# Optimization experiments

Measured on AMD Instinct MI355X. Metric: run time of the kernel, lower is better.

Reference implementation:

```python
import jax, jax.numpy as jnp
import numpy as np

N_NODES = 100_000
N_EDGES = 3_200_000
F_IN, F_HID, F_OUT = 128, 128, 64
BN_EPS = 1e-5


def gcn_conv(x, src, dst, W, b, n_nodes):
    """PyG GCNConv: x' = D^{-1/2}(A+I)D^{-1/2} (x W) + b, self-loops included in src/dst."""
    h = x @ W                                                  # [N, out]
    ones = jnp.ones(src.shape[0], dtype=x.dtype)
    deg = jax.ops.segment_sum(ones, dst, num_segments=n_nodes)  # in-degree incl. self-loop (>=1)
    dinv = jax.lax.rsqrt(deg)
    norm = dinv[src] * dinv[dst]                               # [E+N]
    msg = h[src] * norm[:, None]                               # gather + scale
    out = jax.ops.segment_sum(msg, dst, num_segments=n_nodes)  # scatter-add
    return out + b


def setup_inputs() -> dict:
    key = jax.random.key(0)
    ks = jax.random.split(key, 6)
    x = jax.random.normal(ks[0], (N_NODES, F_IN), dtype=jnp.float32)
    edge_index = jax.random.randint(ks[1], (2, N_EDGES), 0, N_NODES, dtype=jnp.int32)
    W1 = jax.random.normal(ks[2], (F_IN, F_HID), dtype=jnp.float32) / np.sqrt(F_IN)
    b1 = jnp.zeros((F_HID,), dtype=jnp.float32)
    gamma = jnp.ones((F_HID,), dtype=jnp.float32)
    beta = jnp.zeros((F_HID,), dtype=jnp.float32)
    W2 = jax.random.normal(ks[3], (F_HID, F_OUT), dtype=jnp.float32) / np.sqrt(F_HID)
    b2 = jnp.zeros((F_OUT,), dtype=jnp.float32)
    return {"x": x, "edge_index": edge_index, "W1": W1, "b1": b1,
            "gamma": gamma, "beta": beta, "W2": W2, "b2": b2}


def reference(x, edge_index, W1, b1, gamma, beta, W2, b2):
    n = x.shape[0]
    loop = jnp.arange(n, dtype=edge_index.dtype)
    src = jnp.concatenate([edge_index[0], loop])
    dst = jnp.concatenate([edge_index[1], loop])
    # conv1
    h = gcn_conv(x, src, dst, W1, b1, n)
    # BatchNorm1d (training mode: batch stats, biased variance)
    mean = jnp.mean(h, axis=0)
    var = jnp.mean((h - mean) ** 2, axis=0)
    h = (h - mean) * jax.lax.rsqrt(var + BN_EPS) * gamma + beta
    # ReLU
    h = jax.nn.relu(h)
    # conv2
    return gcn_conv(h, src, dst, W2, b2, n)
```

## Files before the change

### kernel.cpp

```cpp
#include <hip/hip_runtime.h>
#include <math.h>


typedef _Float16 f16;
typedef _Float16 f16x2 __attribute__((ext_vector_type(2)));
typedef _Float16 f16x8 __attribute__((ext_vector_type(8)));
typedef float f32x4 __attribute__((ext_vector_type(4)));

static constexpr int KDIM = 128;
static constexpr int MAXNB = 1600;
static constexpr int CAP = 2560;
static constexpr int CHUNK = 8192;
static constexpr int BINT = 512;
static constexpr int WTP = 136;

__global__ __launch_bounds__(BINT) void binA_kernel(
    const int* __restrict__ src, const int* __restrict__ dst, int E,
    int* __restrict__ bcur, unsigned int* __restrict__ bins, int nbuck) {
  __shared__ int hist[MAXNB];
  __shared__ int base[MAXNB];
  const int tid = threadIdx.x;
  for (int b = tid; b < nbuck; b += BINT) hist[b] = 0;
  __syncthreads();
  const int e0 = blockIdx.x * CHUNK;
  const int e1 = min(e0 + CHUNK, E);
  for (int e = e0 + tid * 4; e + 3 < e1; e += BINT * 4) {
    int4 d4 = *reinterpret_cast<const int4*>(&dst[e]);
    atomicAdd(&hist[d4.x >> 6], 1);
    atomicAdd(&hist[d4.y >> 6], 1);
    atomicAdd(&hist[d4.z >> 6], 1);
    atomicAdd(&hist[d4.w >> 6], 1);
  }
  for (int e = e1 - (e1 - e0) % 4 + tid; e < e1; e += BINT) atomicAdd(&hist[dst[e] >> 6], 1);
  __syncthreads();
  for (int b = tid; b < nbuck; b += BINT) {
    int c = hist[b];
    base[b] = c ? atomicAdd(&bcur[b], c) : 0;
    hist[b] = 0;
  }
  __syncthreads();
  for (int e = e0 + tid * 4; e + 3 < e1; e += BINT * 4) {
    int4 d4 = *reinterpret_cast<const int4*>(&dst[e]);
    int4 s4 = *reinterpret_cast<const int4*>(&src[e]);
    int dd[4] = {d4.x, d4.y, d4.z, d4.w};
    int ss[4] = {s4.x, s4.y, s4.z, s4.w};
#pragma unroll
    for (int k = 0; k < 4; ++k) {
      int b = dd[k] >> 6;
      int lp = atomicAdd(&hist[b], 1);
      int p = base[b] + lp;
      if (p < CAP)
        bins[(size_t)b * CAP + p] =
            (unsigned int)ss[k] | ((unsigned int)(dd[k] & 63) << 17);
    }
  }
  for (int e = e1 - (e1 - e0) % 4 + tid; e < e1; e += BINT) {
    int d = dst[e];
    int b = d >> 6;
    int lp = atomicAdd(&hist[b], 1);
    int p = base[b] + lp;
    if (p < CAP)
      bins[(size_t)b * CAP + p] = (unsigned int)src[e] | ((unsigned int)(d & 63) << 17);
  }
}

__global__ __launch_bounds__(1024) void bscan_kernel(
    const int* __restrict__ bcur, int nbuck, int* __restrict__ bbase,
    int* __restrict__ off_n, f16* __restrict__ h1rown) {
  __shared__ int sh[1024];
  const int t = threadIdx.x;
  if (t < 128) h1rown[t] = (f16)0.f;
  int a = (2 * t < nbuck) ? min(bcur[2 * t], CAP) : 0;
  int b = (2 * t + 1 < nbuck) ? min(bcur[2 * t + 1], CAP) : 0;
  sh[t] = a + b;
  __syncthreads();
  for (int o = 1; o < 1024; o <<= 1) {
    int v = (t >= o) ? sh[t - o] : 0;
    __syncthreads();
    sh[t] += v;
    __syncthreads();
  }
  int excl = (t > 0) ? sh[t - 1] : 0;
  if (2 * t < nbuck) bbase[2 * t] = excl;
  if (2 * t + 1 < nbuck) bbase[2 * t + 1] = excl + a;
  if (t == 1023) off_n[0] = sh[1023];
}

__global__ __launch_bounds__(256) void csrfill_kernel(
    const unsigned int* __restrict__ bins, const int* __restrict__ bcur,
    const int* __restrict__ bbase, int* __restrict__ csr, int* __restrict__ off,
    float* __restrict__ dinv, int n) {
  __shared__ int hist[64];
  __shared__ int pref[64];
  __shared__ int lcur[64];
  const int tid = threadIdx.x;
  const int b = blockIdx.x;
  const int cnt = min(bcur[b], CAP);
  const unsigned int* bp = bins + (size_t)b * CAP;
  if (tid < 64) hist[tid] = 0;
  __syncthreads();
  for (int e = tid; e < cnt; e += 256) atomicAdd(&hist[bp[e] >> 17], 1);
  __syncthreads();
  if (tid < 64) pref[tid] = hist[tid];
  __syncthreads();
  for (int o = 1; o < 64; o <<= 1) {
    int v = (tid < 64 && tid >= o) ? pref[tid - o] : 0;
    __syncthreads();
    if (tid < 64) pref[tid] += v;
    __syncthreads();
  }
  if (tid < 64) {
    int node = b * 64 + tid;
    if (node < n) {
      int excl = bbase[b] + pref[tid] - hist[tid];
      off[node] = excl;
      lcur[tid] = excl;
      dinv[node] = rsqrtf((float)(hist[tid] + 1));
    }
  }
  __syncthreads();
  for (int e = tid; e < cnt; e += 256) {
    unsigned int pk = bp[e];
    int r = pk >> 17;
    int p = atomicAdd(&lcur[r], 1);
    csr[p] = (int)(pk & 0x1FFFF);
  }
}

__global__ __launch_bounds__(256) void gemm1_kernel(
    const float* __restrict__ A, const float* __restrict__ W, f16* __restrict__ C,
    int M, const float* __restrict__ dinv) {
  __shared__ f16 Wt[128][WTP];
  const int tid = threadIdx.x;
  for (int idx = tid; idx < 128 * 128; idx += 256) {
    int k = idx >> 7, nn = idx & 127;
    Wt[nn][k] = (f16)W[idx];
  }
  __syncthreads();
  const int wave = tid >> 6;
  const int lane = tid & 63;
  const int r = lane & 15;
  const int kg = lane >> 4;
  const int row0 = blockIdx.x * 64 + wave * 16;
  const bool valid = (row0 + r) < M;
  const float* arow = A + (size_t)(row0 + r) * KDIM;
  f32x4 acc[8];
#pragma unroll
  for (int nf = 0; nf < 8; ++nf) acc[nf] = (f32x4){0.f, 0.f, 0.f, 0.f};
#pragma unroll
  for (int ks = 0; ks < 4; ++ks) {
    const int k0 = ks * 32 + kg * 8;
    f16x8 a;
#pragma unroll
    for (int z = 0; z < 8; ++z) a[z] = (f16)0.f;
    if (valid) {
      float4 u = *reinterpret_cast<const float4*>(arow + k0);
      float4 v = *reinterpret_cast<const float4*>(arow + k0 + 4);
      a[0] = (f16)u.x; a[1] = (f16)u.y; a[2] = (f16)u.z; a[3] = (f16)u.w;
      a[4] = (f16)v.x; a[5] = (f16)v.y; a[6] = (f16)v.z; a[7] = (f16)v.w;
    }
#pragma unroll
    for (int nf = 0; nf < 8; ++nf) {
      f16x8 b = *reinterpret_cast<const f16x8*>(&Wt[nf * 16 + r][k0]);
      acc[nf] = __builtin_amdgcn_mfma_f32_16x16x32_f16(a, b, acc[nf], 0, 0, 0);
    }
  }
  const int crow = row0 + (lane >> 4) * 4;
  const int ccol = lane & 15;
#pragma unroll
  for (int q = 0; q < 4; ++q) {
    int rr = crow + q;
    if (rr < M) {
      float dv = dinv[rr];
#pragma unroll
      for (int nf = 0; nf < 8; ++nf)
        C[(size_t)rr * 128 + nf * 16 + ccol] = (f16)(acc[nf][q] * dv);
    }
  }
}

__global__ __launch_bounds__(256) void gemm2_kernel(
    const f16* __restrict__ A, const float* __restrict__ W, f16* __restrict__ C,
    int M, const float* __restrict__ ss, const float* __restrict__ dinv) {
  __shared__ f16 Wt[64][WTP];
  const int tid = threadIdx.x;
  for (int idx = tid; idx < 128 * 64; idx += 256) {
    int k = idx >> 6, nn = idx & 63;
    Wt[nn][k] = (f16)W[idx];
  }
  __syncthreads();
  const int wave = tid >> 6;
  const int lane = tid & 63;
  const int r = lane & 15;
  const int kg = lane >> 4;
  const int row0 = blockIdx.x * 64 + wave * 16;
  const bool valid = (row0 + r) < M;
  const f16* arow = A + (size_t)(row0 + r) * KDIM;
  f32x4 acc[4];
#pragma unroll
  for (int nf = 0; nf < 4; ++nf) acc[nf] = (f32x4){0.f, 0.f, 0.f, 0.f};
#pragma unroll
  for (int ks = 0; ks < 4; ++ks) {
    const int k0 = ks * 32 + kg * 8;
    f16x8 a;
#pragma unroll
    for (int z = 0; z < 8; ++z) a[z] = (f16)0.f;
    if (valid) {
      f16x8 raw = *reinterpret_cast<const f16x8*>(arow + k0);
      float4 s0 = *reinterpret_cast<const float4*>(&ss[k0]);
      float4 s1 = *reinterpret_cast<const float4*>(&ss[k0 + 4]);
      float4 t0 = *reinterpret_cast<const float4*>(&ss[128 + k0]);
      float4 t1 = *reinterpret_cast<const float4*>(&ss[128 + k0 + 4]);
      a[0] = (f16)fmaxf((float)raw[0] * s0.x + t0.x, 0.f);
      a[1] = (f16)fmaxf((float)raw[1] * s0.y + t0.y, 0.f);
      a[2] = (f16)fmaxf((float)raw[2] * s0.z + t0.z, 0.f);
      a[3] = (f16)fmaxf((float)raw[3] * s0.w + t0.w, 0.f);
      a[4] = (f16)fmaxf((float)raw[4] * s1.x + t1.x, 0.f);
      a[5] = (f16)fmaxf((float)raw[5] * s1.y + t1.y, 0.f);
      a[6] = (f16)fmaxf((float)raw[6] * s1.z + t1.z, 0.f);
      a[7] = (f16)fmaxf((float)raw[7] * s1.w + t1.w, 0.f);
    }
#pragma unroll
    for (int nf = 0; nf < 4; ++nf) {
      f16x8 b = *reinterpret_cast<const f16x8*>(&Wt[nf * 16 + r][k0]);
      acc[nf] = __builtin_amdgcn_mfma_f32_16x16x32_f16(a, b, acc[nf], 0, 0, 0);
    }
  }
  const int crow = row0 + (lane >> 4) * 4;
  const int ccol = lane & 15;
#pragma unroll
  for (int q = 0; q < 4; ++q) {
    int rr = crow + q;
    if (rr < M) {
      float dv = dinv[rr];
#pragma unroll
      for (int nf = 0; nf < 4; ++nf)
        C[(size_t)rr * 64 + nf * 16 + ccol] = (f16)(acc[nf][q] * dv);
    }
  }
}

__global__ __launch_bounds__(64) void agg1_kernel(
    const f16* __restrict__ h, const float* __restrict__ dinv,
    const int* __restrict__ off, const int* __restrict__ csr,
    const float* __restrict__ bias, f16* __restrict__ outh, int n) {
  const int i = blockIdx.x;
  const int t = threadIdx.x;
  const float di = dinv[i];
  const float2 bi = *reinterpret_cast<const float2*>(&bias[2 * t]);
  f16x2 hs = *reinterpret_cast<const f16x2*>(&h[(size_t)i * 128 + 2 * t]);
  float e0 = (float)hs[0];
  float e1 = (float)hs[1];
  const int beg = __builtin_amdgcn_readfirstlane(off[i]);
  const int end = __builtin_amdgcn_readfirstlane(off[i + 1]);
  for (int j = beg & ~15; j < end; j += 16) {
    int4 q0 = *reinterpret_cast<const int4*>(&csr[j]);
    int4 q1 = *reinterpret_cast<const int4*>(&csr[j + 4]);
    int4 q2 = *reinterpret_cast<const int4*>(&csr[j + 8]);
    int4 q3 = *reinterpret_cast<const int4*>(&csr[j + 12]);
    int s[16] = {q0.x, q0.y, q0.z, q0.w, q1.x, q1.y, q1.z, q1.w,
                 q2.x, q2.y, q2.z, q2.w, q3.x, q3.y, q3.z, q3.w};
    if (j < beg || j + 16 > end) {
#pragma unroll
      for (int k = 0; k < 16; ++k)
        if (j + k < beg || j + k >= end) s[k] = n;
    }
    f16x2 v[16];
#pragma unroll
    for (int k = 0; k < 16; ++k)
      v[k] = *reinterpret_cast<const f16x2*>(&h[(size_t)s[k] * 128 + 2 * t]);
#pragma unroll
    for (int k = 0; k < 16; ++k) {
      e0 += (float)v[k][0];
      e1 += (float)v[k][1];
    }
  }
  f16x2 o;
  o[0] = (f16)(di * e0 + bi.x);
  o[1] = (f16)(di * e1 + bi.y);
  *reinterpret_cast<f16x2*>(&outh[(size_t)i * 128 + 2 * t]) = o;
}

__global__ __launch_bounds__(64) void agg2_kernel(
    const f16* __restrict__ h, const float* __restrict__ dinv,
    const int* __restrict__ off, const int* __restrict__ csr,
    const float* __restrict__ bias, float* __restrict__ out, int n) {
  const int i = blockIdx.x;
  const int lane = threadIdx.x;
  const int epar = lane >> 5;
  const int cp = lane & 31;
  const float di = dinv[i];
  float e0 = 0.f, e1 = 0.f;
  const int beg = __builtin_amdgcn_readfirstlane(off[i]);
  const int end = __builtin_amdgcn_readfirstlane(off[i + 1]);
  for (int j = beg & ~15; j < end; j += 16) {
    int4 q0 = *reinterpret_cast<const int4*>(&csr[j]);
    int4 q1 = *reinterpret_cast<const int4*>(&csr[j + 4]);
    int4 q2 = *reinterpret_cast<const int4*>(&csr[j + 8]);
    int4 q3 = *reinterpret_cast<const int4*>(&csr[j + 12]);
    int s[16] = {q0.x, q0.y, q0.z, q0.w, q1.x, q1.y, q1.z, q1.w,
                 q2.x, q2.y, q2.z, q2.w, q3.x, q3.y, q3.z, q3.w};
    if (j < beg || j + 16 > end) {
#pragma unroll
      for (int k = 0; k < 16; ++k)
        if (j + k < beg || j + k >= end) s[k] = n;
    }
#pragma unroll
    for (int k = 0; k < 8; ++k) {
      int se = epar ? s[2 * k + 1] : s[2 * k];
      f16x2 v = *reinterpret_cast<const f16x2*>(&h[(size_t)se * 64 + 2 * cp]);
      e0 += (float)v[0];
      e1 += (float)v[1];
    }
  }
  e0 += __shfl_xor(e0, 32, 64);
  e1 += __shfl_xor(e1, 32, 64);
  if (epar == 0) {
    f16x2 hv = *reinterpret_cast<const f16x2*>(&h[(size_t)i * 64 + 2 * cp]);
    float2 bi = *reinterpret_cast<const float2*>(&bias[2 * cp]);
    float2 o;
    o.x = di * (e0 + (float)hv[0]) + bi.x;
    o.y = di * (e1 + (float)hv[1]) + bi.y;
    *reinterpret_cast<float2*>(&out[(size_t)i * 64 + 2 * cp]) = o;
  }
}

__global__ __launch_bounds__(256) void bnstat_kernel(
    const f16* __restrict__ a, int n, float* __restrict__ acc) {
  __shared__ float sh[16][16][16];
  const int cgrp = threadIdx.x & 15;
  const int rgrp = threadIdx.x >> 4;
  float s[8], ss[8];
#pragma unroll
  for (int z = 0; z < 8; ++z) { s[z] = 0.f; ss[z] = 0.f; }
  for (int r = blockIdx.x * 16 + rgrp; r < n; r += gridDim.x * 16) {
    f16x8 v = *reinterpret_cast<const f16x8*>(&a[(size_t)r * 128 + cgrp * 8]);
#pragma unroll
    for (int z = 0; z < 8; ++z) {
      float f = (float)v[z];
      s[z] += f;
      ss[z] += f * f;
    }
  }
#pragma unroll
  for (int z = 0; z < 8; ++z) {
    sh[rgrp][cgrp][z] = s[z];
    sh[rgrp][cgrp][8 + z] = ss[z];
  }
  __syncthreads();
  const int cg = threadIdx.x >> 4;
  const int zs = threadIdx.x & 15;
  float tot = 0.f;
#pragma unroll
  for (int rg = 0; rg < 16; ++rg) tot += sh[rg][cg][zs];
  if (zs < 8)
    atomicAdd(&acc[cg * 8 + zs], tot);
  else
    atomicAdd(&acc[128 + cg * 8 + (zs - 8)], tot);
}

__global__ void bnfin_kernel(const float* __restrict__ acc, const float* __restrict__ gamma,
                             const float* __restrict__ beta, int n, float* __restrict__ ss,
                             f16* __restrict__ h2rown) {
  const int c = threadIdx.x;
  if (c < 64) h2rown[c] = (f16)0.f;
  const float inv_n = 1.f / (float)n;
  const float mean = acc[c] * inv_n;
  const float var = acc[128 + c] * inv_n - mean * mean;
  const float sc = gamma[c] * rsqrtf(var + 1e-5f);
  ss[c] = sc;
  ss[128 + c] = beta[c] - mean * sc;
}

extern "C" void kernel_launch(void* const* d_in, const int* in_sizes, int n_in,
                              void* d_out, int out_size, void* d_ws, size_t ws_size,
                              hipStream_t stream) {
  const float* x = (const float*)d_in[0];
  const int* ei = (const int*)d_in[1];
  const float* W1 = (const float*)d_in[2];
  const float* b1 = (const float*)d_in[3];
  const float* gamma = (const float*)d_in[4];
  const float* beta = (const float*)d_in[5];
  const float* W2 = (const float*)d_in[6];
  const float* b2 = (const float*)d_in[7];
  float* out = (float*)d_out;

  const int n = in_sizes[0] / 128;
  const int E = in_sizes[1] / 2;
  const int* src = ei;
  const int* dst = ei + E;
  const int nbuck = (n + 63) / 64;

  char* p = (char*)d_ws;
  auto carve = [&](size_t bytes) {
    char* r = p;
    p += (bytes + 255) & ~(size_t)255;
    return r;
  };
  int* bcur = (int*)carve((size_t)nbuck * 4);
  float* bnacc = (float*)carve(256 * 4);
  const size_t zero_bytes = (size_t)((char*)(bnacc + 256) - (char*)bcur);
  int* bbase = (int*)carve((size_t)(nbuck + 1) * 4);
  float* bnss = (float*)carve(256 * 4);
  int* off = (int*)carve((size_t)(n + 1) * 4);
  float* dinv = (float*)carve((size_t)n * 4);
  unsigned int* bins = (unsigned int*)carve((size_t)nbuck * CAP * 4);
  int* csr = (int*)carve((size_t)(E + 64) * 4);
  f16* h1 = (f16*)carve((size_t)(n + 1) * 128 * 2);
  f16* agg1 = (f16*)carve((size_t)n * 128 * 2);
  f16* h2 = h1;

  hipMemsetAsync(bcur, 0, zero_bytes, stream);

  const int ngb = (n + 63) / 64;

  binA_kernel<<<(E + CHUNK - 1) / CHUNK, BINT, 0, stream>>>(src, dst, E, bcur, bins, nbuck);
  bscan_kernel<<<1, 1024, 0, stream>>>(bcur, nbuck, bbase, off + n, h1 + (size_t)n * 128);
  csrfill_kernel<<<nbuck, 256, 0, stream>>>(bins, bcur, bbase, csr, off, dinv, n);

  gemm1_kernel<<<ngb, 256, 0, stream>>>(x, W1, h1, n, dinv);
  agg1_kernel<<<n, 64, 0, stream>>>(h1, dinv, off, csr, b1, agg1, n);

  bnstat_kernel<<<512, 256, 0, stream>>>(agg1, n, bnacc);
  bnfin_kernel<<<1, 128, 0, stream>>>(bnacc, gamma, beta, n, bnss, h2 + (size_t)n * 64);

  gemm2_kernel<<<ngb, 256, 0, stream>>>(agg1, W2, h2, n, bnss, dinv);
  agg2_kernel<<<n, 64, 0, stream>>>(h2, dinv, off, csr, b2, out, n);
}
```

Before: 302.2 us.

## Enlarge binning chunks, split CSR fill counters, and double gemm1 rows per block

Doubles the binning chunk size and block size, so fewer blocks each take a larger share of edges. In the CSR fill, the per-node histogram and cursor atomics are split into four sub-counters, which lowers shared-memory atomic contention. gemm1 now covers 128 rows per block with two row tiles per wave, so each block's transposed-W staging in LDS is reused over more rows. The trade-offs are more registers per thread and fewer blocks in flight; CSR order within a node also changes, which can change floating-point summation order.

```diff
diff --git a/kernel.cpp b/kernel.cpp
--- a/kernel.cpp
+++ b/kernel.cpp
@@ -10,8 +10,8 @@
 static constexpr int KDIM = 128;
 static constexpr int MAXNB = 1600;
 static constexpr int CAP = 2560;
-static constexpr int CHUNK = 8192;
-static constexpr int BINT = 512;
+static constexpr int CHUNK = 16384;
+static constexpr int BINT = 1024;
 static constexpr int WTP = 136;
 
 __global__ __launch_bounds__(BINT) void binA_kernel(
@@ -90,18 +90,23 @@
     const unsigned int* __restrict__ bins, const int* __restrict__ bcur,
     const int* __restrict__ bbase, int* __restrict__ csr, int* __restrict__ off,
     float* __restrict__ dinv, int n) {
-  __shared__ int hist[64];
+  __shared__ int hist2[64][4];
   __shared__ int pref[64];
-  __shared__ int lcur[64];
+  __shared__ int lcur2[64][4];
   const int tid = threadIdx.x;
+  const int sub = tid & 3;
   const int b = blockIdx.x;
   const int cnt = min(bcur[b], CAP);
   const unsigned int* bp = bins + (size_t)b * CAP;
-  if (tid < 64) hist[tid] = 0;
-  __syncthreads();
-  for (int e = tid; e < cnt; e += 256) atomicAdd(&hist[bp[e] >> 17], 1);
-  __syncthreads();
-  if (tid < 64) pref[tid] = hist[tid];
+  hist2[tid >> 2][tid & 3] = 0;
+  __syncthreads();
+  for (int e = tid; e < cnt; e += 256) atomicAdd(&hist2[bp[e] >> 17][sub], 1);
+  __syncthreads();
+  int tot = 0;
+  if (tid < 64) {
+    tot = hist2[tid][0] + hist2[tid][1] + hist2[tid][2] + hist2[tid][3];
+    pref[tid] = tot;
+  }
   __syncthreads();
   for (int o = 1; o < 64; o <<= 1) {
     int v = (tid < 64 && tid >= o) ? pref[tid - o] : 0;
@@ -112,17 +117,20 @@
   if (tid < 64) {
     int node = b * 64 + tid;
     if (node < n) {
-      int excl = bbase[b] + pref[tid] - hist[tid];
+      int excl = bbase[b] + pref[tid] - tot;
       off[node] = excl;
-      lcur[tid] = excl;
-      dinv[node] = rsqrtf((float)(hist[tid] + 1));
+      lcur2[tid][0] = excl;
+      lcur2[tid][1] = excl + hist2[tid][0];
+      lcur2[tid][2] = excl + hist2[tid][0] + hist2[tid][1];
+      lcur2[tid][3] = excl + hist2[tid][0] + hist2[tid][1] + hist2[tid][2];
+      dinv[node] = rsqrtf((float)(tot + 1));
     }
   }
   __syncthreads();
   for (int e = tid; e < cnt; e += 256) {
     unsigned int pk = bp[e];
     int r = pk >> 17;
-    int p = atomicAdd(&lcur[r], 1);
+    int p = atomicAdd(&lcur2[r][sub], 1);
     csr[p] = (int)(pk & 0x1FFFF);
   }
 }
@@ -141,40 +149,48 @@
   const int lane = tid & 63;
   const int r = lane & 15;
   const int kg = lane >> 4;
-  const int row0 = blockIdx.x * 64 + wave * 16;
-  const bool valid = (row0 + r) < M;
-  const float* arow = A + (size_t)(row0 + r) * KDIM;
-  f32x4 acc[8];
-#pragma unroll
-  for (int nf = 0; nf < 8; ++nf) acc[nf] = (f32x4){0.f, 0.f, 0.f, 0.f};
+  f32x4 acc[2][8];
+#pragma unroll
+  for (int rt = 0; rt < 2; ++rt)
+#pragma unroll
+    for (int nf = 0; nf < 8; ++nf) acc[rt][nf] = (f32x4){0.f, 0.f, 0.f, 0.f};
+  const int rbase = blockIdx.x * 128 + wave * 16;
 #pragma unroll
   for (int ks = 0; ks < 4; ++ks) {
     const int k0 = ks * 32 + kg * 8;
-    f16x8 a;
-#pragma unroll
-    for (int z = 0; z < 8; ++z) a[z] = (f16)0.f;
-    if (valid) {
-      float4 u = *reinterpret_cast<const float4*>(arow + k0);
-      float4 v = *reinterpret_cast<const float4*>(arow + k0 + 4);
-      a[0] = (f16)u.x; a[1] = (f16)u.y; a[2] = (f16)u.z; a[3] = (f16)u.w;
-      a[4] = (f16)v.x; a[5] = (f16)v.y; a[6] = (f16)v.z; a[7] = (f16)v.w;
-    }
-#pragma unroll
-    for (int nf = 0; nf < 8; ++nf) {
-      f16x8 b = *reinterpret_cast<const f16x8*>(&Wt[nf * 16 + r][k0]);
-      acc[nf] = __builtin_amdgcn_mfma_f32_16x16x32_f16(a, b, acc[nf], 0, 0, 0);
-    }
-  }
-  const int crow = row0 + (lane >> 4) * 4;
+#pragma unroll
+    for (int rt = 0; rt < 2; ++rt) {
+      const int row0 = rbase + rt * 64;
+      f16x8 a;
+#pragma unroll
+      for (int z = 0; z < 8; ++z) a[z] = (f16)0.f;
+      if (row0 + r < M) {
+        const float* arow = A + (size_t)(row0 + r) * KDIM;
+        float4 u = *reinterpret_cast<const float4*>(arow + k0);
+        float4 v = *reinterpret_cast<const float4*>(arow + k0 + 4);
+        a[0] = (f16)u.x; a[1] = (f16)u.y; a[2] = (f16)u.z; a[3] = (f16)u.w;
+        a[4] = (f16)v.x; a[5] = (f16)v.y; a[6] = (f16)v.z; a[7] = (f16)v.w;
+      }
+#pragma unroll
+      for (int nf = 0; nf < 8; ++nf) {
+        f16x8 b = *reinterpret_cast<const f16x8*>(&Wt[nf * 16 + r][k0]);
+        acc[rt][nf] = __builtin_amdgcn_mfma_f32_16x16x32_f16(a, b, acc[rt][nf], 0, 0, 0);
+      }
+    }
+  }
   const int ccol = lane & 15;
 #pragma unroll
-  for (int q = 0; q < 4; ++q) {
-    int rr = crow + q;
-    if (rr < M) {
-      float dv = dinv[rr];
-#pragma unroll
-      for (int nf = 0; nf < 8; ++nf)
-        C[(size_t)rr * 128 + nf * 16 + ccol] = (f16)(acc[nf][q] * dv);
+  for (int rt = 0; rt < 2; ++rt) {
+    const int crow = rbase + rt * 64 + (lane >> 4) * 4;
+#pragma unroll
+    for (int q = 0; q < 4; ++q) {
+      int rr = crow + q;
+      if (rr < M) {
+        float dv = dinv[rr];
+#pragma unroll
+        for (int nf = 0; nf < 8; ++nf)
+          C[(size_t)rr * 128 + nf * 16 + ccol] = (f16)(acc[rt][nf][q] * dv);
+      }
     }
   }
 }
@@ -412,18 +428,16 @@
 
   hipMemsetAsync(bcur, 0, zero_bytes, stream);
 
-  const int ngb = (n + 63) / 64;
-
   binA_kernel<<<(E + CHUNK - 1) / CHUNK, BINT, 0, stream>>>(src, dst, E, bcur, bins, nbuck);
   bscan_kernel<<<1, 1024, 0, stream>>>(bcur, nbuck, bbase, off + n, h1 + (size_t)n * 128);
   csrfill_kernel<<<nbuck, 256, 0, stream>>>(bins, bcur, bbase, csr, off, dinv, n);
 
-  gemm1_kernel<<<ngb, 256, 0, stream>>>(x, W1, h1, n, dinv);
+  gemm1_kernel<<<(n + 127) / 128, 256, 0, stream>>>(x, W1, h1, n, dinv);
   agg1_kernel<<<n, 64, 0, stream>>>(h1, dinv, off, csr, b1, agg1, n);
 
   bnstat_kernel<<<512, 256, 0, stream>>>(agg1, n, bnacc);
   bnfin_kernel<<<1, 128, 0, stream>>>(bnacc, gamma, beta, n, bnss, h2 + (size_t)n * 64);
 
-  gemm2_kernel<<<ngb, 256, 0, stream>>>(agg1, W2, h2, n, bnss, dinv);
+  gemm2_kernel<<<(n + 63) / 64, 256, 0, stream>>>(agg1, W2, h2, n, bnss, dinv);
   agg2_kernel<<<n, 64, 0, stream>>>(h2, dinv, off, csr, b2, out, n);
 }
```

Result: no change. 298.4 us (-1.2%).
